# Optimization experiments

Hardware: AMD Instinct MI355X
Metric: run time of the kernel (lower is better)

## Reference

```python
import jax, jax.numpy as jnp
import numpy as np

B, NPG = 128, 128          # graphs, nodes per graph
N = B * NPG                # total nodes
K = 16                     # kNN neighbors within cutoff
D = 256                    # embedding_depth
H, DH = 4, 32              # heads = num_layers, head dim = (D//2)//H
L = 4                      # num graph convolutions
NR = 50                    # num_radial
CUTOFF = 2.0
OUT = 3 + 100              # 3 + max_ntypes


def setup_inputs() -> dict:
    rng = np.random.default_rng(0)
    pos = rng.standard_normal((N, 3)).astype(np.float32)
    nbrs = np.zeros((N, K), np.int32)
    mask = np.zeros((N, K), np.float32)
    for g in range(B):  # per-graph kNN with radial cutoff (setup only, numpy)
        p = pos[g * NPG:(g + 1) * NPG]
        d2 = ((p[:, None, :] - p[None, :, :]) ** 2).sum(-1)
        np.fill_diagonal(d2, np.inf)
        idx = np.argsort(d2, axis=1)[:, :K]
        dk = np.sqrt(np.take_along_axis(d2, idx, 1))
        nbrs[g * NPG:(g + 1) * NPG] = idx + g * NPG
        mask[g * NPG:(g + 1) * NPG] = (dk <= CUTOFF).astype(np.float32)
    batch_idx = np.repeat(np.arange(B, dtype=np.int32), NPG)

    key = jax.random.key(0)
    ks = jax.random.split(key, 12)
    s = 0.02
    return {
        'encoding': jax.random.normal(ks[0], (B, D), jnp.float32),
        'pos': jnp.asarray(pos),
        'batch_idx': jnp.asarray(batch_idx),
        'neighbors': jnp.asarray(nbrs),
        'nbr_mask': jnp.asarray(mask),
        'W_in': jax.random.normal(ks[1], (D + 3, D), jnp.float32) * s,
        'b_in': jnp.zeros((D,), jnp.float32),
        'Wq': jax.random.normal(ks[2], (L, D, H * DH), jnp.float32) * s,
        'Wk': jax.random.normal(ks[3], (L, D, H * DH), jnp.float32) * s,
        'Wv': jax.random.normal(ks[4], (L, D, H * DH), jnp.float32) * s,
        'We': jax.random.normal(ks[5], (L, NR, H * DH), jnp.float32) * s,
        'Wo': jax.random.normal(ks[6], (L, H * DH, D), jnp.float32) * s,
        'bo': jnp.zeros((L, D), jnp.float32),
        'Wfc': jax.random.normal(ks[7], (L, D, D), jnp.float32) * s,
        'bfc': jnp.zeros((L, D), jnp.float32),
        'ln_g': jnp.ones((L, D), jnp.float32),
        'ln_b': jnp.zeros((L, D), jnp.float32),
        'W_out': jax.random.normal(ks[8], (D, OUT), jnp.float32) * s,
        'b_out': jnp.zeros((OUT,), jnp.float32),
    }


def reference(encoding, pos, batch_idx, neighbors, nbr_mask,
              W_in, b_in, Wq, Wk, Wv, We, Wo, bo, Wfc, bfc,
              ln_g, ln_b, W_out, b_out):
    # x = encoding.repeat_interleave(graph_sizes); x[:, 0] = 1
    x = encoding[batch_idx]                      # [N, D]
    x = x.at[:, 0].set(1.0)
    h = jnp.concatenate([x, pos], axis=-1) @ W_in + b_in   # concat pos, embed

    # gaussian radial basis of neighbor distances
    dvec = pos[neighbors] - pos[:, None, :]      # [N, K, 3]
    d = jnp.sqrt((dvec ** 2).sum(-1) + 1e-12)    # [N, K]
    centers = jnp.linspace(0.0, CUTOFF, NR)
    width = centers[1] - centers[0]
    rbf = jnp.exp(-0.5 * ((d[..., None] - centers) / width) ** 2)  # [N, K, NR]

    scale = 1.0 / jnp.sqrt(jnp.float32(DH))
    m = nbr_mask[..., None]                      # [N, K, 1]
    for l in range(L):                           # TransformerConv layers
        q = (h @ Wq[l]).reshape(N, H, DH)
        k = (h @ Wk[l]).reshape(N, H, DH)
        v = (h @ Wv[l]).reshape(N, H, DH)
        e = (rbf @ We[l]).reshape(N, K, H, DH)   # edge embedding
        kj = k[neighbors] + e                    # [N, K, H, DH]
        vj = v[neighbors] + e
        logits = jnp.einsum('nhd,nkhd->nkh', q, kj) * scale
        logits = jnp.where(m > 0, logits, -1e9)
        a = jax.nn.softmax(logits, axis=1) * m   # masked attention over K
        msg = jnp.einsum('nkh,nkhd->nhd', a, vj).reshape(N, H * DH)
        h = h + msg @ Wo[l] + bo[l]              # residual update
        mu = h.mean(-1, keepdims=True)
        var = h.var(-1, keepdims=True)
        h = ln_g[l] * (h - mu) / jnp.sqrt(var + 1e-5) + ln_b[l]
        h = jax.nn.gelu(h @ Wfc[l] + bfc[l])     # nodewise fc (1 layer)

    return h @ W_out + b_out                     # [N, 3 + max_ntypes]
```

## Files before the change

### kernel.cpp

```cpp
#include <hip/hip_runtime.h>
#include <hip/hip_bf16.h>
#include <math.h>

#define N_PTS 16384
#define NLAYER 4

typedef __attribute__((ext_vector_type(8))) short bfrag;
typedef __attribute__((ext_vector_type(4))) float f32x4;
typedef __attribute__((ext_vector_type(4))) unsigned short u16x4;
typedef unsigned short ushort_t;
typedef unsigned int uint_t;

__device__ __forceinline__ ushort_t f2b(float f) {
  __hip_bfloat16 h = __float2bfloat16(f);
  return *reinterpret_cast<const ushort_t*>(&h);
}
__device__ __forceinline__ float b2f(ushort_t u) {
  union { uint_t i; float f; } c; c.i = ((uint_t)u) << 16; return c.f;
}
__device__ __forceinline__ float blo(uint_t u) {
  union { uint_t i; float f; } c; c.i = u << 16; return c.f;
}
__device__ __forceinline__ float bhi(uint_t u) {
  union { uint_t i; float f; } c; c.i = u & 0xffff0000u; return c.f;
}

__device__ __forceinline__ void gload16(const ushort_t* g, ushort_t* l) {
  __builtin_amdgcn_global_load_lds(
      (const __attribute__((address_space(1))) unsigned int*)g,
      (__attribute__((address_space(3))) unsigned int*)l, 16, 0, 0);
}

__global__ __launch_bounds__(256) void base_kernel(
    const float* __restrict__ enc, const float* __restrict__ W_in,
    const float* __restrict__ b_in, float* __restrict__ base)
{
  int b = blockIdx.x, j = threadIdx.x;
  __shared__ float se[256];
  se[j] = enc[b * 256 + j];
  __syncthreads();
  float acc = b_in[j] + W_in[j];
  for (int i = 1; i < 256; ++i) acc += se[i] * W_in[i * 256 + j];
  base[b * 256 + j] = acc;
}

__global__ __launch_bounds__(256) void embed_kernel(
    const float* __restrict__ base, const int* __restrict__ batch_idx,
    const float* __restrict__ pos, const float* __restrict__ W_in,
    float* __restrict__ h, ushort_t* __restrict__ h_bf)
{
  int n = blockIdx.x, j = threadIdx.x;
  int b = batch_idx[n];
  float px = pos[n * 3 + 0], py = pos[n * 3 + 1], pz = pos[n * 3 + 2];
  float v = base[b * 256 + j]
      + px * W_in[256 * 256 + j] + py * W_in[257 * 256 + j] + pz * W_in[258 * 256 + j];
  h[(size_t)n * 256 + j] = v;
  h_bf[(size_t)n * 256 + j] = f2b(v);
}

__global__ __launch_bounds__(256) void prep_qkv(
    const float* __restrict__ Wq, const float* __restrict__ Wk,
    const float* __restrict__ Wv, const float* __restrict__ We,
    ushort_t* __restrict__ out)
{
  int idx = blockIdx.x * 256 + threadIdx.x;
  int l = idx / (640 * 256);
  int rem = idx - l * (640 * 256);
  int j = rem >> 8, k = rem & 255;
  float v = 0.f;
  if (j < 128) v = Wq[((size_t)l * 256 + k) * 128 + j];
  else if (j < 328) {
    int p = j - 128, hq = p / 50, r = p - hq * 50;
    const float* wq = &Wq[((size_t)l * 256 + k) * 128 + hq * 32];
    const float* we = &We[((size_t)l * 50 + r) * 128 + hq * 32];
#pragma unroll
    for (int d = 0; d < 32; ++d) v += wq[d] * we[d];
  } else if (j < 456) v = Wk[((size_t)l * 256 + k) * 128 + (j - 328)];
  else if (j < 584) v = Wv[((size_t)l * 256 + k) * 128 + (j - 456)];
  out[idx] = f2b(v);
}

__global__ __launch_bounds__(256) void prep_bcat(
    const float* __restrict__ We, const float* __restrict__ Wo, ushort_t* __restrict__ out)
{
  int idx = blockIdx.x * 256 + threadIdx.x;
  if (idx >= 4 * 256 * 352) return;
  int l = idx / (256 * 352);
  int rem = idx - l * (256 * 352);
  int j = rem / 352, k2 = rem - j * 352;
  float v = 0.f;
  if (k2 < 128) v = Wo[((size_t)l * 128 + k2) * 256 + j];
  else if (k2 < 328) {
    int p = k2 - 128, hq = p / 50, r = p - hq * 50;
    const float* we = &We[((size_t)l * 50 + r) * 128 + hq * 32];
    const float* wo = &Wo[((size_t)l * 128 + hq * 32) * 256 + j];
#pragma unroll
    for (int d = 0; d < 32; ++d) v += we[d] * wo[(size_t)d * 256];
  }
  out[idx] = f2b(v);
}

__global__ __launch_bounds__(256) void prep_wfc(
    const float* __restrict__ Wfc, ushort_t* __restrict__ out)
{
  int idx = blockIdx.x * 256 + threadIdx.x;
  int l = idx >> 16, rem = idx & 65535;
  int j = rem >> 8, k = rem & 255;
  out[idx] = f2b(Wfc[((size_t)l * 256 + k) * 256 + j]);
}

__global__ __launch_bounds__(256) void prep_wout(
    const float* __restrict__ W_out, ushort_t* __restrict__ out)
{
  int idx = blockIdx.x * 256 + threadIdx.x;
  int j = idx >> 8, k = idx & 255;
  out[idx] = (j < 103) ? f2b(W_out[(size_t)k * 103 + j]) : (ushort_t)0;
}

template<int EPI>
__global__ __launch_bounds__(256) void gemm_bf16(
    const ushort_t* __restrict__ A, const ushort_t* __restrict__ BT,
    const float* __restrict__ bias,
    float* __restrict__ Cf, ushort_t* __restrict__ Cb, ushort_t* __restrict__ Cb2,
    int K)
{
  __shared__ __align__(16) ushort_t As[128 * 32];
  __shared__ __align__(16) ushort_t Bs[128 * 32];
  const int tid = threadIdx.x;
  const int m0 = blockIdx.x * 128, n0 = blockIdx.y * 128;
  const int lane = tid & 63, wv = tid >> 6;
  const int wm = wv >> 1, wn = wv & 1;
  const int l15 = lane & 15, l4 = lane >> 4;

  const int srow = wv * 16 + (lane >> 2);
  const int skc = (lane & 3) << 3;
  const ushort_t* gA0 = A + (size_t)(m0 + srow) * K + skc;
  const ushort_t* gA1 = gA0 + (size_t)64 * K;
  const ushort_t* gB0 = BT + (size_t)(n0 + srow) * K + skc;
  const ushort_t* gB1 = gB0 + (size_t)64 * K;
  ushort_t* lA0 = As + wv * 512;
  ushort_t* lA1 = As + 2048 + wv * 512;
  ushort_t* lB0 = Bs + wv * 512;
  ushort_t* lB1 = Bs + 2048 + wv * 512;

  f32x4 acc[4][4];
#pragma unroll
  for (int i = 0; i < 4; ++i)
#pragma unroll
    for (int j = 0; j < 4; ++j) acc[i][j] = (f32x4){0.f, 0.f, 0.f, 0.f};

  for (int k0 = 0; k0 < K; k0 += 32) {
    gload16(gA0 + k0, lA0);
    gload16(gA1 + k0, lA1);
    gload16(gB0 + k0, lB0);
    gload16(gB1 + k0, lB1);
    __syncthreads();
    bfrag af[4], bf[4];
#pragma unroll
    for (int m = 0; m < 4; ++m)
      af[m] = *(const bfrag*)(As + (wm * 64 + m * 16 + l15) * 32 + l4 * 8);
#pragma unroll
    for (int nn = 0; nn < 4; ++nn)
      bf[nn] = *(const bfrag*)(Bs + (wn * 64 + nn * 16 + l15) * 32 + l4 * 8);
#pragma unroll
    for (int m = 0; m < 4; ++m)
#pragma unroll
      for (int nn = 0; nn < 4; ++nn)
        acc[m][nn] = __builtin_amdgcn_mfma_f32_16x16x32_bf16(af[m], bf[nn], acc[m][nn], 0, 0, 0);
    __syncthreads();
  }

#pragma unroll
  for (int m = 0; m < 4; ++m) {
    const int rbase = m0 + wm * 64 + m * 16 + l4 * 4;
#pragma unroll
    for (int nn = 0; nn < 4; ++nn) {
      const int c = n0 + wn * 64 + nn * 16 + l15;
#pragma unroll
      for (int i = 0; i < 4; ++i) {
        const int r = rbase + i;
        float v = acc[m][nn][i];
        if (EPI == 0) {
          if (c < 328) Cb[(size_t)r * 328 + c] = f2b(v);
          else if (c < 584) Cb2[(size_t)r * 256 + (c - 328)] = f2b(v);
        } else if (EPI == 1) {
          if (c < 103) Cf[(size_t)r * 103 + c] = v + bias[c];
        } else {
          float x = v + bias[c];
          float t = tanhf(0.7978845608028654f * (x + 0.044715f * x * x * x));
          float gl = 0.5f * x * (1.f + t);
          Cf[(size_t)r * 256 + c] = gl;
          Cb[(size_t)r * 256 + c] = f2b(gl);
        }
      }
    }
  }
}

__global__ __launch_bounds__(512) void gemm_woln(
    const ushort_t* __restrict__ A, const ushort_t* __restrict__ BT,
    const float* __restrict__ bo, const float* __restrict__ resid,
    const float* __restrict__ lgm, const float* __restrict__ lbt,
    ushort_t* __restrict__ hln)
{
  __shared__ __align__(16) ushort_t As[64 * 32];
  __shared__ __align__(16) ushort_t Bs[256 * 32];
  __shared__ float pS[8][64], pSS[8][64];
  const int tid = threadIdx.x;
  const int lane = tid & 63, w = tid >> 6;
  const int l15 = lane & 15, l4 = lane >> 4;
  const int m0 = blockIdx.x * 64;
  const int K = 352;

  const int srow = lane >> 2, skc = (lane & 3) << 3;
  const ushort_t* gA = A + (size_t)(m0 + w * 16 + srow) * K + skc;
  const ushort_t* gB0 = BT + (size_t)((w * 2 + 0) * 16 + srow) * K + skc;
  const ushort_t* gB1 = BT + (size_t)((w * 2 + 1) * 16 + srow) * K + skc;
  ushort_t* lA = As + w * 512;
  ushort_t* lB0 = Bs + (w * 2 + 0) * 512;
  ushort_t* lB1 = Bs + (w * 2 + 1) * 512;

  f32x4 acc[4][2];
#pragma unroll
  for (int i = 0; i < 4; ++i) {
    acc[i][0] = (f32x4){0.f, 0.f, 0.f, 0.f};
    acc[i][1] = (f32x4){0.f, 0.f, 0.f, 0.f};
  }

  for (int k0 = 0; k0 < K; k0 += 32) {
    if (w < 4) gload16(gA + k0, lA);
    gload16(gB0 + k0, lB0);
    gload16(gB1 + k0, lB1);
    __syncthreads();
    bfrag af[4], bf[2];
#pragma unroll
    for (int m = 0; m < 4; ++m)
      af[m] = *(const bfrag*)(As + (m * 16 + l15) * 32 + l4 * 8);
#pragma unroll
    for (int nn = 0; nn < 2; ++nn)
      bf[nn] = *(const bfrag*)(Bs + (w * 32 + nn * 16 + l15) * 32 + l4 * 8);
#pragma unroll
    for (int m = 0; m < 4; ++m)
#pragma unroll
      for (int nn = 0; nn < 2; ++nn)
        acc[m][nn] = __builtin_amdgcn_mfma_f32_16x16x32_bf16(af[m], bf[nn], acc[m][nn], 0, 0, 0);
    __syncthreads();
  }

  const int c0 = w * 32 + l15;
  const int c1 = c0 + 16;
  const float bo0 = bo[c0], bo1 = bo[c1];
  const float g0 = lgm[c0], g1 = lgm[c1];
  const float b0 = lbt[c0], b1 = lbt[c1];

#pragma unroll
  for (int m = 0; m < 4; ++m) {
#pragma unroll
    for (int i = 0; i < 4; ++i) {
      const int rl = m * 16 + l4 * 4 + i;
      const size_t r = (size_t)(m0 + rl);
      float x0 = acc[m][0][i] + bo0 + resid[r * 256 + c0];
      float x1 = acc[m][1][i] + bo1 + resid[r * 256 + c1];
      acc[m][0][i] = x0; acc[m][1][i] = x1;
      float s = x0 + x1, ss = x0 * x0 + x1 * x1;
      s += __shfl_xor(s, 1, 64); ss += __shfl_xor(ss, 1, 64);
      s += __shfl_xor(s, 2, 64); ss += __shfl_xor(ss, 2, 64);
      s += __shfl_xor(s, 4, 64); ss += __shfl_xor(ss, 4, 64);
      s += __shfl_xor(s, 8, 64); ss += __shfl_xor(ss, 8, 64);
      if (l15 == 0) { pS[w][rl] = s; pSS[w][rl] = ss; }
    }
  }
  __syncthreads();
#pragma unroll
  for (int m = 0; m < 4; ++m) {
#pragma unroll
    for (int i = 0; i < 4; ++i) {
      const int rl = m * 16 + l4 * 4 + i;
      float s = 0.f, ss = 0.f;
#pragma unroll
      for (int w2 = 0; w2 < 8; ++w2) { s += pS[w2][rl]; ss += pSS[w2][rl]; }
      float mu = s * (1.f / 256.f);
      float var = ss * (1.f / 256.f) - mu * mu;
      float inv = 1.0f / sqrtf(var + 1e-5f);
      const size_t r = (size_t)(m0 + rl);
      hln[r * 256 + c0] = f2b(g0 * (acc[m][0][i] - mu) * inv + b0);
      hln[r * 256 + c1] = f2b(g1 * (acc[m][1][i] - mu) * inv + b1);
    }
  }
}

__global__ __launch_bounds__(256) void attn_kernel(
    const ushort_t* __restrict__ qext, const ushort_t* __restrict__ kvb,
    const float* __restrict__ pos, const int* __restrict__ nbrs,
    const float* __restrict__ mask, ushort_t* __restrict__ Amsg)
{
  __shared__ __align__(16) ushort_t sQ[4][128];
  __shared__ __align__(16) float    sQE[4][4][52];
  __shared__ __align__(16) ushort_t sRbf[4][16][52];
  __shared__ float sA[4][64];
  __shared__ float sD[4][16];
  __shared__ float sMk[4][16];
  __shared__ int   sNb[4][16];

  const int tid = threadIdx.x;
  const int lane = tid & 63, w = tid >> 6;
  const int g = blockIdx.x & 127, q4 = blockIdx.x >> 7;
  const int kk = lane >> 2, hh = lane & 3;

  for (int it = 0; it < 4; ++it) {
    const int n = g * 128 + q4 * 16 + w * 4 + it;
    if (lane < 16) {
      int nb = nbrs[n * 16 + lane];
      sNb[w][lane] = nb;
      sMk[w][lane] = mask[n * 16 + lane];
      float dx = pos[nb * 3 + 0] - pos[n * 3 + 0];
      float dy = pos[nb * 3 + 1] - pos[n * 3 + 1];
      float dz = pos[nb * 3 + 2] - pos[n * 3 + 2];
      sD[w][lane] = sqrtf(dx * dx + dy * dy + dz * dz + 1e-12f);
      sRbf[w][lane][50] = 0; sRbf[w][lane][51] = 0;
      *(uint4*)(&sQ[w][lane * 8]) = *(const uint4*)(qext + (size_t)n * 328 + lane * 8);
    }
    if (lane < 50) {
      uint2 u = *(const uint2*)(qext + (size_t)n * 328 + 128 + lane * 4);
      int p = lane * 4;
#pragma unroll
      for (int e = 0; e < 4; ++e) {
        ushort_t bb = ((const ushort_t*)&u)[e];
        int pp = p + e, h2 = pp / 50, r = pp - h2 * 50;
        sQE[w][h2][r] = b2f(bb);
      }
    }
    if (lane < 8) sQE[w][lane >> 1][50 + (lane & 1)] = 0.f;
    {
      int kk2 = lane & 15;
      float dk = sD[w][kk2];
      int r0 = lane >> 4;
#pragma unroll
      for (int j = 0; j < 13; ++j) {
        int r = r0 + j * 4;
        if (r < 50) {
          float t = (dk - (2.f / 49.f) * (float)r) * 24.5f;
          sRbf[w][kk2][r] = f2b(__expf(-0.5f * t * t));
        }
      }
    }
    const int nb = sNb[w][kk];
    const ushort_t* krow = kvb + (size_t)nb * 256 + hh * 32;
    float qk = 0.f;
#pragma unroll
    for (int c8 = 0; c8 < 4; ++c8) {
      uint4 kv4 = *(const uint4*)(krow + c8 * 8);
      const uint_t* q4p = (const uint_t*)(&sQ[w][hh * 32 + c8 * 8]);
      uint_t qa = q4p[0], qb = q4p[1], qc = q4p[2], qd = q4p[3];
      qk += blo(qa) * blo(kv4.x) + bhi(qa) * bhi(kv4.x)
          + blo(qb) * blo(kv4.y) + bhi(qb) * bhi(kv4.y)
          + blo(qc) * blo(kv4.z) + bhi(qc) * bhi(kv4.z)
          + blo(qd) * blo(kv4.w) + bhi(qd) * bhi(kv4.w);
    }
    float qe = 0.f;
#pragma unroll
    for (int c = 0; c < 13; ++c) {
      float4 qv = *(const float4*)(&sQE[w][hh][c * 4]);
      uint2 rv = *(const uint2*)(&sRbf[w][kk][c * 4]);
      qe += qv.x * blo(rv.x) + qv.y * bhi(rv.x)
          + qv.z * blo(rv.y) + qv.w * bhi(rv.y);
    }
    float lg = 0.17677669529663687f * (qk + qe);
    lg = (sMk[w][kk] > 0.f) ? lg : -1e9f;

    float mx = lg;
#pragma unroll
    for (int off = 4; off < 64; off <<= 1) mx = fmaxf(mx, __shfl_xor(mx, off, 64));
    float ex = __expf(lg - mx);
    float sm = ex;
#pragma unroll
    for (int off = 4; off < 64; off <<= 1) sm += __shfl_xor(sm, off, 64);
    sA[w][kk * 4 + hh] = ex / sm * sMk[w][kk];

    if (lane < 50) {
      float r0 = 0.f, r1 = 0.f, r2 = 0.f, r3 = 0.f;
#pragma unroll
      for (int k2 = 0; k2 < 16; ++k2) {
        float rb = b2f(sRbf[w][k2][lane]);
        r0 += sA[w][k2 * 4 + 0] * rb;
        r1 += sA[w][k2 * 4 + 1] * rb;
        r2 += sA[w][k2 * 4 + 2] * rb;
        r3 += sA[w][k2 * 4 + 3] * rb;
      }
      Amsg[(size_t)n * 352 + 128 + 0 * 50 + lane] = f2b(r0);
      Amsg[(size_t)n * 352 + 128 + 1 * 50 + lane] = f2b(r1);
      Amsg[(size_t)n * 352 + 128 + 2 * 50 + lane] = f2b(r2);
      Amsg[(size_t)n * 352 + 128 + 3 * 50 + lane] = f2b(r3);
    }
    {
      const int h2 = lane >> 4;
      float m0v = 0.f, m1v = 0.f;
#pragma unroll
      for (int k2 = 0; k2 < 16; ++k2) {
        int nb2 = sNb[w][k2];
        uint_t vv = *(const uint_t*)(kvb + (size_t)nb2 * 256 + 128 + lane * 2);
        float a = sA[w][k2 * 4 + h2];
        m0v += a * blo(vv);
        m1v += a * bhi(vv);
      }
      uint_t o = (uint_t)f2b(m0v) | ((uint_t)f2b(m1v) << 16);
      *(uint_t*)(&Amsg[(size_t)n * 352 + lane * 2]) = o;
    }
    if (lane < 24) Amsg[(size_t)n * 352 + 328 + lane] = 0;
  }
}

extern "C" void kernel_launch(void* const* d_in, const int* in_sizes, int n_in,
                              void* d_out, int out_size, void* d_ws, size_t ws_size,
                              hipStream_t stream) {
  const float* enc    = (const float*)d_in[0];
  const float* pos    = (const float*)d_in[1];
  const int*   bidx   = (const int*)  d_in[2];
  const int*   nbrs   = (const int*)  d_in[3];
  const float* mask   = (const float*)d_in[4];
  const float* W_in   = (const float*)d_in[5];
  const float* b_in   = (const float*)d_in[6];
  const float* Wq     = (const float*)d_in[7];
  const float* Wk     = (const float*)d_in[8];
  const float* Wv     = (const float*)d_in[9];
  const float* We     = (const float*)d_in[10];
  const float* Wo     = (const float*)d_in[11];
  const float* bo     = (const float*)d_in[12];
  const float* Wfc    = (const float*)d_in[13];
  const float* bfc    = (const float*)d_in[14];
  const float* ln_g   = (const float*)d_in[15];
  const float* ln_b   = (const float*)d_in[16];
  const float* W_out  = (const float*)d_in[17];
  const float* b_out  = (const float*)d_in[18];
  float* out = (float*)d_out;

  const int N = N_PTS;
  float* ws = (float*)d_ws;
  float*    h      = ws;
  ushort_t* qext_b = (ushort_t*)(h + (size_t)N * 256);
  ushort_t* kvb    = qext_b + (size_t)N * 328;
  ushort_t* hln    = kvb;
  ushort_t* h_bf   = kvb + (size_t)N * 256;
  ushort_t* Amsg   = h_bf + (size_t)N * 256;
  float*    base   = (float*)(Amsg + (size_t)N * 352);
  ushort_t* WqkvT  = (ushort_t*)(base + 128 * 256);
  ushort_t* BcT    = WqkvT + 4 * 640 * 256;
  ushort_t* WfT    = BcT  + 4 * 256 * 352;
  ushort_t* WoT    = WfT  + 4 * 256 * 256;

  base_kernel<<<128, 256, 0, stream>>>(enc, W_in, b_in, base);
  embed_kernel<<<N, 256, 0, stream>>>(base, bidx, pos, W_in, h, h_bf);
  prep_qkv<<<(4 * 640 * 256) / 256, 256, 0, stream>>>(Wq, Wk, Wv, We, WqkvT);
  prep_bcat<<<(4 * 256 * 352 + 255) / 256, 256, 0, stream>>>(We, Wo, BcT);
  prep_wfc<<<(4 * 256 * 256) / 256, 256, 0, stream>>>(Wfc, WfT);
  prep_wout<<<(128 * 256) / 256, 256, 0, stream>>>(W_out, WoT);

  for (int l = 0; l < NLAYER; ++l) {
    const ushort_t* WqkvT_l = WqkvT + (size_t)l * 640 * 256;
    const ushort_t* BcT_l   = BcT   + (size_t)l * 256 * 352;
    const ushort_t* WfT_l   = WfT   + (size_t)l * 256 * 256;
    const float* bo_l  = bo  + (size_t)l * 256;
    const float* bfc_l = bfc + (size_t)l * 256;
    const float* lg_l  = ln_g + (size_t)l * 256;
    const float* lb_l  = ln_b + (size_t)l * 256;

    gemm_bf16<0><<<dim3(N / 128, 5), 256, 0, stream>>>(
        h_bf, WqkvT_l, nullptr, nullptr, qext_b, kvb, 256);

    attn_kernel<<<1024, 256, 0, stream>>>(qext_b, kvb, pos, nbrs, mask, Amsg);

    gemm_woln<<<N / 64, 512, 0, stream>>>(
        Amsg, BcT_l, bo_l, h, lg_l, lb_l, hln);

    gemm_bf16<3><<<dim3(N / 128, 2), 256, 0, stream>>>(
        hln, WfT_l, bfc_l, h, h_bf, nullptr, 256);
  }

  gemm_bf16<1><<<dim3(N / 128, 1), 256, 0, stream>>>(
      h_bf, WoT, b_out, out, nullptr, nullptr, 256);
}
```

Measured before the change: 374.6 us.

## Fuse Wo+LayerNorm, FC+GELU and next-layer QKV GEMM into one kernel

Replaces the separate Wo+LN GEMM, the FC+GELU GEMM and the next layer's QKV GEMM with a single per-64-row kernel that keeps intermediates (LN output, GELU output) in shared memory. The final layer also fuses the output projection. This removes the global round-trips of hln and h_bf and several launches. Weight tiles use XOR-swizzled LDS layouts and the padded K is raised to 384 and qext stride to 352. The cost is larger LDS use, which limits occupancy, and the QKV weights get reloaded per block over 5 column chunks.

```diff
diff --git a/kernel.cpp b/kernel.cpp
--- a/kernel.cpp
+++ b/kernel.cpp
@@ -84,10 +84,9 @@
     const float* __restrict__ We, const float* __restrict__ Wo, ushort_t* __restrict__ out)
 {
   int idx = blockIdx.x * 256 + threadIdx.x;
-  if (idx >= 4 * 256 * 352) return;
-  int l = idx / (256 * 352);
-  int rem = idx - l * (256 * 352);
-  int j = rem / 352, k2 = rem - j * 352;
+  int l = idx / (256 * 384);
+  int rem = idx - l * (256 * 384);
+  int j = rem / 384, k2 = rem - j * 384;
   float v = 0.f;
   if (k2 < 128) v = Wo[((size_t)l * 128 + k2) * 256 + j];
   else if (k2 < 328) {
@@ -117,175 +116,225 @@
   out[idx] = (j < 103) ? f2b(W_out[(size_t)k * 103 + j]) : (ushort_t)0;
 }
 
-template<int EPI>
-__global__ __launch_bounds__(256) void gemm_bf16(
-    const ushort_t* __restrict__ A, const ushort_t* __restrict__ BT,
-    const float* __restrict__ bias,
-    float* __restrict__ Cf, ushort_t* __restrict__ Cb, ushort_t* __restrict__ Cb2,
-    int K)
-{
-  __shared__ __align__(16) ushort_t As[128 * 32];
-  __shared__ __align__(16) ushort_t Bs[128 * 32];
-  const int tid = threadIdx.x;
-  const int m0 = blockIdx.x * 128, n0 = blockIdx.y * 128;
-  const int lane = tid & 63, wv = tid >> 6;
-  const int wm = wv >> 1, wn = wv & 1;
-  const int l15 = lane & 15, l4 = lane >> 4;
-
-  const int srow = wv * 16 + (lane >> 2);
-  const int skc = (lane & 3) << 3;
-  const ushort_t* gA0 = A + (size_t)(m0 + srow) * K + skc;
-  const ushort_t* gA1 = gA0 + (size_t)64 * K;
-  const ushort_t* gB0 = BT + (size_t)(n0 + srow) * K + skc;
-  const ushort_t* gB1 = gB0 + (size_t)64 * K;
-  ushort_t* lA0 = As + wv * 512;
-  ushort_t* lA1 = As + 2048 + wv * 512;
-  ushort_t* lB0 = Bs + wv * 512;
-  ushort_t* lB1 = Bs + 2048 + wv * 512;
-
-  f32x4 acc[4][4];
-#pragma unroll
-  for (int i = 0; i < 4; ++i)
-#pragma unroll
-    for (int j = 0; j < 4; ++j) acc[i][j] = (f32x4){0.f, 0.f, 0.f, 0.f};
-
-  for (int k0 = 0; k0 < K; k0 += 32) {
-    gload16(gA0 + k0, lA0);
-    gload16(gA1 + k0, lA1);
-    gload16(gB0 + k0, lB0);
-    gload16(gB1 + k0, lB1);
-    __syncthreads();
-    bfrag af[4], bf[4];
-#pragma unroll
-    for (int m = 0; m < 4; ++m)
-      af[m] = *(const bfrag*)(As + (wm * 64 + m * 16 + l15) * 32 + l4 * 8);
-#pragma unroll
-    for (int nn = 0; nn < 4; ++nn)
-      bf[nn] = *(const bfrag*)(Bs + (wn * 64 + nn * 16 + l15) * 32 + l4 * 8);
-#pragma unroll
-    for (int m = 0; m < 4; ++m)
-#pragma unroll
-      for (int nn = 0; nn < 4; ++nn)
-        acc[m][nn] = __builtin_amdgcn_mfma_f32_16x16x32_bf16(af[m], bf[nn], acc[m][nn], 0, 0, 0);
-    __syncthreads();
-  }
-
-#pragma unroll
-  for (int m = 0; m < 4; ++m) {
-    const int rbase = m0 + wm * 64 + m * 16 + l4 * 4;
-#pragma unroll
-    for (int nn = 0; nn < 4; ++nn) {
-      const int c = n0 + wn * 64 + nn * 16 + l15;
-#pragma unroll
-      for (int i = 0; i < 4; ++i) {
-        const int r = rbase + i;
-        float v = acc[m][nn][i];
-        if (EPI == 0) {
-          if (c < 328) Cb[(size_t)r * 328 + c] = f2b(v);
-          else if (c < 584) Cb2[(size_t)r * 256 + (c - 328)] = f2b(v);
-        } else if (EPI == 1) {
-          if (c < 103) Cf[(size_t)r * 103 + c] = v + bias[c];
-        } else {
-          float x = v + bias[c];
-          float t = tanhf(0.7978845608028654f * (x + 0.044715f * x * x * x));
-          float gl = 0.5f * x * (1.f + t);
-          Cf[(size_t)r * 256 + c] = gl;
-          Cb[(size_t)r * 256 + c] = f2b(gl);
-        }
-      }
-    }
-  }
-}
-
-__global__ __launch_bounds__(512) void gemm_woln(
-    const ushort_t* __restrict__ A, const ushort_t* __restrict__ BT,
-    const float* __restrict__ bo, const float* __restrict__ resid,
-    const float* __restrict__ lgm, const float* __restrict__ lbt,
-    ushort_t* __restrict__ hln)
-{
-  __shared__ __align__(16) ushort_t As[64 * 32];
-  __shared__ __align__(16) ushort_t Bs[256 * 32];
+template<int MODE>
+__global__ __launch_bounds__(512, 2) void fused_layer(
+    const ushort_t* __restrict__ A0,
+    const ushort_t* __restrict__ BcT,
+    const float* __restrict__ bo,
+    float* __restrict__ h,
+    const float* __restrict__ lg, const float* __restrict__ lb,
+    const ushort_t* __restrict__ WfT,
+    const float* __restrict__ bfc,
+    const ushort_t* __restrict__ W3T,
+    const float* __restrict__ b3,
+    ushort_t* __restrict__ qext_b, ushort_t* __restrict__ kvb,
+    float* __restrict__ outF)
+{
+  __shared__ __align__(16) ushort_t R0[64 * 392];
+  __shared__ __align__(16) ushort_t R12[64 * 264 + 256 * 64];
   __shared__ float pS[8][64], pSS[8][64];
+  ushort_t* sA  = R0;
+  ushort_t* sHg = R0;
+  ushort_t* sH  = R12;
+  ushort_t* sB  = R12 + 64 * 264;
+  ushort_t* B3  = R12;
+
   const int tid = threadIdx.x;
   const int lane = tid & 63, w = tid >> 6;
   const int l15 = lane & 15, l4 = lane >> 4;
   const int m0 = blockIdx.x * 64;
-  const int K = 352;
-
-  const int srow = lane >> 2, skc = (lane & 3) << 3;
-  const ushort_t* gA = A + (size_t)(m0 + w * 16 + srow) * K + skc;
-  const ushort_t* gB0 = BT + (size_t)((w * 2 + 0) * 16 + srow) * K + skc;
-  const ushort_t* gB1 = BT + (size_t)((w * 2 + 1) * 16 + srow) * K + skc;
-  ushort_t* lA = As + w * 512;
-  ushort_t* lB0 = Bs + (w * 2 + 0) * 512;
-  ushort_t* lB1 = Bs + (w * 2 + 1) * 512;
+  const int swzk = (l15 & 7) << 3;
 
   f32x4 acc[4][2];
-#pragma unroll
-  for (int i = 0; i < 4; ++i) {
-    acc[i][0] = (f32x4){0.f, 0.f, 0.f, 0.f};
-    acc[i][1] = (f32x4){0.f, 0.f, 0.f, 0.f};
-  }
-
-  for (int k0 = 0; k0 < K; k0 += 32) {
-    if (w < 4) gload16(gA + k0, lA);
-    gload16(gB0 + k0, lB0);
-    gload16(gB1 + k0, lB1);
+
+  if constexpr (MODE != 2) {
+    for (int i = tid; i < 64 * 48; i += 512) {
+      int r = i / 48, cc = (i - r * 48) * 8;
+      uint4 v = (uint4){0, 0, 0, 0};
+      if (cc < 352) v = *(const uint4*)(A0 + (size_t)(m0 + r) * 352 + cc);
+      *(uint4*)(&sA[r * 392 + cc]) = v;
+    }
+
+#pragma unroll
+    for (int m = 0; m < 4; ++m) {
+      acc[m][0] = (f32x4){0.f, 0.f, 0.f, 0.f};
+      acc[m][1] = (f32x4){0.f, 0.f, 0.f, 0.f};
+    }
+    for (int ks = 0; ks < 6; ++ks) {
+      const int k0 = ks * 64;
+#pragma unroll
+      for (int it = 0; it < 4; ++it) {
+        int chunk = it * 512 + tid;
+        int row = chunk >> 3;
+        int kc = ((chunk & 7) << 3) ^ ((row & 7) << 3);
+        gload16(BcT + (size_t)row * 384 + k0 + kc, sB + (size_t)(it * 512 + w * 64) * 8);
+      }
+      __syncthreads();
+#pragma unroll
+      for (int kk = 0; kk < 64; kk += 32) {
+        bfrag af[4], bf[2];
+#pragma unroll
+        for (int m = 0; m < 4; ++m)
+          af[m] = *(const bfrag*)(sA + (m * 16 + l15) * 392 + k0 + kk + l4 * 8);
+#pragma unroll
+        for (int nn = 0; nn < 2; ++nn) {
+          int row = w * 32 + nn * 16 + l15;
+          bf[nn] = *(const bfrag*)(sB + row * 64 + ((kk + l4 * 8) ^ swzk));
+        }
+#pragma unroll
+        for (int m = 0; m < 4; ++m)
+#pragma unroll
+          for (int nn = 0; nn < 2; ++nn)
+            acc[m][nn] = __builtin_amdgcn_mfma_f32_16x16x32_bf16(af[m], bf[nn], acc[m][nn], 0, 0, 0);
+      }
+      __syncthreads();
+    }
+
+    {
+      const int c0 = w * 32 + l15, c1 = c0 + 16;
+      const float bo0 = bo[c0], bo1 = bo[c1];
+#pragma unroll
+      for (int m = 0; m < 4; ++m)
+#pragma unroll
+        for (int i = 0; i < 4; ++i) {
+          const int rl = m * 16 + l4 * 4 + i;
+          const size_t r = (size_t)(m0 + rl);
+          float x0 = acc[m][0][i] + bo0 + h[r * 256 + c0];
+          float x1 = acc[m][1][i] + bo1 + h[r * 256 + c1];
+          acc[m][0][i] = x0; acc[m][1][i] = x1;
+          float s = x0 + x1, ss = x0 * x0 + x1 * x1;
+          s += __shfl_xor(s, 1, 64); ss += __shfl_xor(ss, 1, 64);
+          s += __shfl_xor(s, 2, 64); ss += __shfl_xor(ss, 2, 64);
+          s += __shfl_xor(s, 4, 64); ss += __shfl_xor(ss, 4, 64);
+          s += __shfl_xor(s, 8, 64); ss += __shfl_xor(ss, 8, 64);
+          if (l15 == 0) { pS[w][rl] = s; pSS[w][rl] = ss; }
+        }
+      __syncthreads();
+      const float g0 = lg[c0], g1 = lg[c1];
+      const float b0 = lb[c0], b1 = lb[c1];
+#pragma unroll
+      for (int m = 0; m < 4; ++m)
+#pragma unroll
+        for (int i = 0; i < 4; ++i) {
+          const int rl = m * 16 + l4 * 4 + i;
+          float s = 0.f, ss = 0.f;
+#pragma unroll
+          for (int w2 = 0; w2 < 8; ++w2) { s += pS[w2][rl]; ss += pSS[w2][rl]; }
+          float mu = s * (1.f / 256.f);
+          float var = ss * (1.f / 256.f) - mu * mu;
+          float inv = 1.0f / sqrtf(var + 1e-5f);
+          sH[rl * 264 + c0] = f2b(g0 * (acc[m][0][i] - mu) * inv + b0);
+          sH[rl * 264 + c1] = f2b(g1 * (acc[m][1][i] - mu) * inv + b1);
+        }
+    }
+
+#pragma unroll
+    for (int m = 0; m < 4; ++m) {
+      acc[m][0] = (f32x4){0.f, 0.f, 0.f, 0.f};
+      acc[m][1] = (f32x4){0.f, 0.f, 0.f, 0.f};
+    }
+    for (int ks = 0; ks < 4; ++ks) {
+      const int k0 = ks * 64;
+#pragma unroll
+      for (int it = 0; it < 4; ++it) {
+        int chunk = it * 512 + tid;
+        int row = chunk >> 3;
+        int kc = ((chunk & 7) << 3) ^ ((row & 7) << 3);
+        gload16(WfT + (size_t)row * 256 + k0 + kc, sB + (size_t)(it * 512 + w * 64) * 8);
+      }
+      __syncthreads();
+#pragma unroll
+      for (int kk = 0; kk < 64; kk += 32) {
+        bfrag af[4], bf[2];
+#pragma unroll
+        for (int m = 0; m < 4; ++m)
+          af[m] = *(const bfrag*)(sH + (m * 16 + l15) * 264 + k0 + kk + l4 * 8);
+#pragma unroll
+        for (int nn = 0; nn < 2; ++nn) {
+          int row = w * 32 + nn * 16 + l15;
+          bf[nn] = *(const bfrag*)(sB + row * 64 + ((kk + l4 * 8) ^ swzk));
+        }
+#pragma unroll
+        for (int m = 0; m < 4; ++m)
+#pragma unroll
+          for (int nn = 0; nn < 2; ++nn)
+            acc[m][nn] = __builtin_amdgcn_mfma_f32_16x16x32_bf16(af[m], bf[nn], acc[m][nn], 0, 0, 0);
+      }
+      __syncthreads();
+    }
+
+    {
+      const int c0 = w * 32 + l15, c1 = c0 + 16;
+      const float bf0 = bfc[c0], bf1 = bfc[c1];
+#pragma unroll
+      for (int m = 0; m < 4; ++m)
+#pragma unroll
+        for (int i = 0; i < 4; ++i) {
+          const int rl = m * 16 + l4 * 4 + i;
+          const size_t r = (size_t)(m0 + rl);
+          float x0 = acc[m][0][i] + bf0;
+          float x1 = acc[m][1][i] + bf1;
+          float t0 = tanhf(0.7978845608028654f * (x0 + 0.044715f * x0 * x0 * x0));
+          float t1 = tanhf(0.7978845608028654f * (x1 + 0.044715f * x1 * x1 * x1));
+          float gl0 = 0.5f * x0 * (1.f + t0);
+          float gl1 = 0.5f * x1 * (1.f + t1);
+          h[r * 256 + c0] = gl0;
+          h[r * 256 + c1] = gl1;
+          sHg[rl * 264 + c0] = f2b(gl0);
+          sHg[rl * 264 + c1] = f2b(gl1);
+        }
+    }
     __syncthreads();
-    bfrag af[4], bf[2];
-#pragma unroll
-    for (int m = 0; m < 4; ++m)
-      af[m] = *(const bfrag*)(As + (m * 16 + l15) * 32 + l4 * 8);
-#pragma unroll
-    for (int nn = 0; nn < 2; ++nn)
-      bf[nn] = *(const bfrag*)(Bs + (w * 32 + nn * 16 + l15) * 32 + l4 * 8);
-#pragma unroll
-    for (int m = 0; m < 4; ++m)
-#pragma unroll
-      for (int nn = 0; nn < 2; ++nn)
-        acc[m][nn] = __builtin_amdgcn_mfma_f32_16x16x32_bf16(af[m], bf[nn], acc[m][nn], 0, 0, 0);
+  } else {
+    for (int i = tid; i < 64 * 32; i += 512) {
+      int r = i >> 5, cc = (i & 31) << 3;
+      *(uint4*)(&sHg[r * 264 + cc]) = *(const uint4*)(A0 + (size_t)(m0 + r) * 256 + cc);
+    }
     __syncthreads();
   }
 
-  const int c0 = w * 32 + l15;
-  const int c1 = c0 + 16;
-  const float bo0 = bo[c0], bo1 = bo[c1];
-  const float g0 = lgm[c0], g1 = lgm[c1];
-  const float b0 = lbt[c0], b1 = lbt[c1];
-
-#pragma unroll
-  for (int m = 0; m < 4; ++m) {
-#pragma unroll
-    for (int i = 0; i < 4; ++i) {
-      const int rl = m * 16 + l4 * 4 + i;
-      const size_t r = (size_t)(m0 + rl);
-      float x0 = acc[m][0][i] + bo0 + resid[r * 256 + c0];
-      float x1 = acc[m][1][i] + bo1 + resid[r * 256 + c1];
-      acc[m][0][i] = x0; acc[m][1][i] = x1;
-      float s = x0 + x1, ss = x0 * x0 + x1 * x1;
-      s += __shfl_xor(s, 1, 64); ss += __shfl_xor(ss, 1, 64);
-      s += __shfl_xor(s, 2, 64); ss += __shfl_xor(ss, 2, 64);
-      s += __shfl_xor(s, 4, 64); ss += __shfl_xor(ss, 4, 64);
-      s += __shfl_xor(s, 8, 64); ss += __shfl_xor(ss, 8, 64);
-      if (l15 == 0) { pS[w][rl] = s; pSS[w][rl] = ss; }
-    }
-  }
-  __syncthreads();
-#pragma unroll
-  for (int m = 0; m < 4; ++m) {
-#pragma unroll
-    for (int i = 0; i < 4; ++i) {
-      const int rl = m * 16 + l4 * 4 + i;
-      float s = 0.f, ss = 0.f;
-#pragma unroll
-      for (int w2 = 0; w2 < 8; ++w2) { s += pS[w2][rl]; ss += pSS[w2][rl]; }
-      float mu = s * (1.f / 256.f);
-      float var = ss * (1.f / 256.f) - mu * mu;
-      float inv = 1.0f / sqrtf(var + 1e-5f);
-      const size_t r = (size_t)(m0 + rl);
-      hln[r * 256 + c0] = f2b(g0 * (acc[m][0][i] - mu) * inv + b0);
-      hln[r * 256 + c1] = f2b(g1 * (acc[m][1][i] - mu) * inv + b1);
-    }
+  const int NB = (MODE == 1) ? 1 : 5;
+  for (int nb = 0; nb < NB; ++nb) {
+    if (nb) __syncthreads();
+#pragma unroll
+    for (int it = 0; it < 8; ++it) {
+      int chunk = it * 512 + tid;
+      int row = chunk >> 5;
+      int kc = ((chunk & 31) << 3) ^ ((row & 7) << 3);
+      gload16(W3T + (size_t)(nb * 128 + row) * 256 + kc, B3 + (size_t)(it * 512 + w * 64) * 8);
+    }
+    __syncthreads();
+    f32x4 a3[4];
+#pragma unroll
+    for (int m = 0; m < 4; ++m) a3[m] = (f32x4){0.f, 0.f, 0.f, 0.f};
+#pragma unroll
+    for (int k0 = 0; k0 < 256; k0 += 32) {
+      bfrag af[4], bf;
+#pragma unroll
+      for (int m = 0; m < 4; ++m)
+        af[m] = *(const bfrag*)(sHg + (m * 16 + l15) * 264 + k0 + l4 * 8);
+      {
+        int row = w * 16 + l15;
+        bf = *(const bfrag*)(B3 + row * 256 + ((k0 + l4 * 8) ^ swzk));
+      }
+#pragma unroll
+      for (int m = 0; m < 4; ++m)
+        a3[m] = __builtin_amdgcn_mfma_f32_16x16x32_bf16(af[m], bf, a3[m], 0, 0, 0);
+    }
+    const int c = nb * 128 + w * 16 + l15;
+#pragma unroll
+    for (int m = 0; m < 4; ++m)
+#pragma unroll
+      for (int i = 0; i < 4; ++i) {
+        const size_t r = (size_t)(m0 + m * 16 + l4 * 4 + i);
+        float v = a3[m][i];
+        if constexpr (MODE == 1) {
+          if (c < 103) outF[r * 103 + c] = v + b3[c];
+        } else {
+          if (c < 328) qext_b[r * 352 + c] = f2b(v);
+          else if (c < 584) kvb[r * 256 + (c - 328)] = f2b(v);
+        }
+      }
   }
 }
 
@@ -318,10 +367,10 @@
       float dz = pos[nb * 3 + 2] - pos[n * 3 + 2];
       sD[w][lane] = sqrtf(dx * dx + dy * dy + dz * dz + 1e-12f);
       sRbf[w][lane][50] = 0; sRbf[w][lane][51] = 0;
-      *(uint4*)(&sQ[w][lane * 8]) = *(const uint4*)(qext + (size_t)n * 328 + lane * 8);
+      *(uint4*)(&sQ[w][lane * 8]) = *(const uint4*)(qext + (size_t)n * 352 + lane * 8);
     }
     if (lane < 50) {
-      uint2 u = *(const uint2*)(qext + (size_t)n * 328 + 128 + lane * 4);
+      uint2 u = *(const uint2*)(qext + (size_t)n * 352 + 128 + lane * 4);
       int p = lane * 4;
 #pragma unroll
       for (int e = 0; e < 4; ++e) {
@@ -438,44 +487,45 @@
   float* ws = (float*)d_ws;
   float*    h      = ws;
   ushort_t* qext_b = (ushort_t*)(h + (size_t)N * 256);
-  ushort_t* kvb    = qext_b + (size_t)N * 328;
-  ushort_t* hln    = kvb;
+  ushort_t* kvb    = qext_b + (size_t)N * 352;
   ushort_t* h_bf   = kvb + (size_t)N * 256;
   ushort_t* Amsg   = h_bf + (size_t)N * 256;
   float*    base   = (float*)(Amsg + (size_t)N * 352);
   ushort_t* WqkvT  = (ushort_t*)(base + 128 * 256);
   ushort_t* BcT    = WqkvT + 4 * 640 * 256;
-  ushort_t* WfT    = BcT  + 4 * 256 * 352;
+  ushort_t* WfT    = BcT  + 4 * 256 * 384;
   ushort_t* WoT    = WfT  + 4 * 256 * 256;
 
   base_kernel<<<128, 256, 0, stream>>>(enc, W_in, b_in, base);
   embed_kernel<<<N, 256, 0, stream>>>(base, bidx, pos, W_in, h, h_bf);
   prep_qkv<<<(4 * 640 * 256) / 256, 256, 0, stream>>>(Wq, Wk, Wv, We, WqkvT);
-  prep_bcat<<<(4 * 256 * 352 + 255) / 256, 256, 0, stream>>>(We, Wo, BcT);
+  prep_bcat<<<(4 * 256 * 384) / 256, 256, 0, stream>>>(We, Wo, BcT);
   prep_wfc<<<(4 * 256 * 256) / 256, 256, 0, stream>>>(Wfc, WfT);
   prep_wout<<<(128 * 256) / 256, 256, 0, stream>>>(W_out, WoT);
 
+  fused_layer<2><<<N / 64, 512, 0, stream>>>(
+      h_bf, nullptr, nullptr, nullptr, nullptr, nullptr, nullptr, nullptr,
+      WqkvT, nullptr, qext_b, kvb, nullptr);
+
   for (int l = 0; l < NLAYER; ++l) {
-    const ushort_t* WqkvT_l = WqkvT + (size_t)l * 640 * 256;
-    const ushort_t* BcT_l   = BcT   + (size_t)l * 256 * 352;
-    const ushort_t* WfT_l   = WfT   + (size_t)l * 256 * 256;
+    const ushort_t* BcT_l = BcT + (size_t)l * 256 * 384;
+    const ushort_t* WfT_l = WfT + (size_t)l * 256 * 256;
     const float* bo_l  = bo  + (size_t)l * 256;
     const float* bfc_l = bfc + (size_t)l * 256;
     const float* lg_l  = ln_g + (size_t)l * 256;
     const float* lb_l  = ln_b + (size_t)l * 256;
 
-    gemm_bf16<0><<<dim3(N / 128, 5), 256, 0, stream>>>(
-        h_bf, WqkvT_l, nullptr, nullptr, qext_b, kvb, 256);
-
     attn_kernel<<<1024, 256, 0, stream>>>(qext_b, kvb, pos, nbrs, mask, Amsg);
 
-    gemm_woln<<<N / 64, 512, 0, stream>>>(
-        Amsg, BcT_l, bo_l, h, lg_l, lb_l, hln);
-
-    gemm_bf16<3><<<dim3(N / 128, 2), 256, 0, stream>>>(
-        hln, WfT_l, bfc_l, h, h_bf, nullptr, 256);
+    if (l < NLAYER - 1) {
+      const ushort_t* Wqkv_next = WqkvT + (size_t)(l + 1) * 640 * 256;
+      fused_layer<0><<<N / 64, 512, 0, stream>>>(
+          Amsg, BcT_l, bo_l, h, lg_l, lb_l, WfT_l, bfc_l,
+          Wqkv_next, nullptr, qext_b, kvb, nullptr);
+    } else {
+      fused_layer<1><<<N / 64, 512, 0, stream>>>(
+          Amsg, BcT_l, bo_l, h, lg_l, lb_l, WfT_l, bfc_l,
+          WoT, b_out, nullptr, nullptr, out);
+    }
   }
-
-  gemm_bf16<1><<<dim3(N / 128, 1), 256, 0, stream>>>(
-      h_bf, WoT, b_out, out, nullptr, nullptr, 256);
-}
+}
```

After: 359.7 us. -4.0%, faster.
